# Performance work log

Measured on AMD Instinct MI355X. Metric: run time of the kernel, lower is better.

The kernel has to match this reference:

```python
import jax, jax.numpy as jnp
import numpy as np
from jax.ops import segment_sum, segment_max

DIM = 32   # hidden dim (hardcoded in Net)
N = 10000  # nodes
E = 160000 # edges
B = 64     # graphs in batch


def setup_inputs():
    key = jax.random.key(0)
    ks = jax.random.split(key, 16)
    r = lambda k, s: jax.random.normal(k, s, dtype=jnp.float32) * 0.1
    z = lambda s: jnp.zeros(s, jnp.float32)
    return {
        "x": jax.random.normal(ks[0], (N, 1), jnp.float32),
        "edge_attr": jax.random.normal(ks[1], (E, 2), jnp.float32),
        "lin0_w": r(ks[2], (1, DIM)), "lin0_b": z((DIM,)),
        "nn_w1": r(ks[3], (2, 128)), "nn_b1": z((128,)),
        "nn_w2": r(ks[4], (128, DIM * DIM)), "nn_b2": z((DIM * DIM,)),
        "conv_root": r(ks[5], (DIM, DIM)), "conv_bias": z((DIM,)),
        "gru_w_ih": r(ks[6], (DIM, 3 * DIM)), "gru_w_hh": r(ks[7], (DIM, 3 * DIM)),
        "gru_b_ih": z((3 * DIM,)), "gru_b_hh": z((3 * DIM,)),
        "lstm_w_ih": r(ks[8], (2 * DIM, 4 * DIM)), "lstm_w_hh": r(ks[9], (DIM, 4 * DIM)),
        "lstm_b_ih": z((4 * DIM,)), "lstm_b_hh": z((4 * DIM,)),
        "lin1_w": r(ks[10], (2 * DIM, DIM)), "lin1_b": z((DIM,)),
        "lin2_w": r(ks[11], (DIM, 1)), "lin2_b": z((1,)),
        "edge_index": jax.random.randint(ks[12], (2, E), 0, N),
        "batch": jnp.sort(jax.random.randint(ks[13], (N,), 0, B)),
    }


def _forward(x, edge_attr, params, edge_index, batch):
    (lin0_w, lin0_b, nn_w1, nn_b1, nn_w2, nn_b2, conv_root, conv_bias,
     gru_w_ih, gru_w_hh, gru_b_ih, gru_b_hh,
     lstm_w_ih, lstm_w_hh, lstm_b_ih, lstm_b_hh,
     lin1_w, lin1_b, lin2_w, lin2_b) = params
    src, dst = edge_index[0], edge_index[1]
    deg = jnp.maximum(segment_sum(jnp.ones((E,), x.dtype), dst, num_segments=N), 1.0)[:, None]
    # edge-conditioned weight matrices (depend only on edge_attr -> compute once)
    ew = (jax.nn.relu(edge_attr @ nn_w1 + nn_b1) @ nn_w2 + nn_b2).reshape(E, DIM, DIM)

    out = jax.nn.relu(x @ lin0_w + lin0_b)  # (N, DIM)
    h = out                                  # GRU hidden state
    for _ in range(3):
        # NNConv: gather -> per-edge matmul -> scatter-mean, plus root weight + bias
        msg = jnp.einsum('ei,eio->eo', out[src], ew)          # (E, DIM)
        agg = segment_sum(msg, dst, num_segments=N) / deg      # (N, DIM)
        m = jax.nn.relu(agg + out @ conv_root + conv_bias)
        # single GRU step (seq_len = 1)
        gi = m @ gru_w_ih + gru_b_ih
        gh = h @ gru_w_hh + gru_b_hh
        i_r, i_z, i_n = jnp.split(gi, 3, axis=-1)
        h_r, h_z, h_n = jnp.split(gh, 3, axis=-1)
        rg = jax.nn.sigmoid(i_r + h_r)
        zg = jax.nn.sigmoid(i_z + h_z)
        ng = jnp.tanh(i_n + rg * h_n)
        h = (1.0 - zg) * ng + zg * h
        out = h

    # Set2Set pooling, 3 processing steps
    q_star = jnp.zeros((B, 2 * DIM), x.dtype)
    hh = jnp.zeros((B, DIM), x.dtype)
    cc = jnp.zeros((B, DIM), x.dtype)
    for _ in range(3):
        gates = q_star @ lstm_w_ih + lstm_b_ih + hh @ lstm_w_hh + lstm_b_hh
        ig, fg, gg, og = jnp.split(gates, 4, axis=-1)  # torch gate order i,f,g,o
        cc = jax.nn.sigmoid(fg) * cc + jax.nn.sigmoid(ig) * jnp.tanh(gg)
        hh = jax.nn.sigmoid(og) * jnp.tanh(cc)
        q = hh                                          # (B, DIM)
        e = jnp.sum(out * q[batch], axis=-1)            # (N,)
        a = jnp.exp(e - segment_max(e, batch, num_segments=B)[batch])
        a = a / segment_sum(a, batch, num_segments=B)[batch]
        rvec = segment_sum(a[:, None] * out, batch, num_segments=B)  # (B, DIM)
        q_star = jnp.concatenate([q, rvec], axis=-1)

    y = jax.nn.relu(q_star @ lin1_w + lin1_b)
    return (y @ lin2_w + lin2_b).reshape(-1)  # (B,)


def reference(x, edge_attr, lin0_w, lin0_b, nn_w1, nn_b1, nn_w2, nn_b2, conv_root, conv_bias, gru_w_ih, gru_w_hh, gru_b_ih, gru_b_hh, lstm_w_ih, lstm_w_hh, lstm_b_ih, lstm_b_hh, lin1_w, lin1_b, lin2_w, lin2_b, edge_index, batch):
    params = (lin0_w, lin0_b, nn_w1, nn_b1, nn_w2, nn_b2, conv_root, conv_bias,
              gru_w_ih, gru_w_hh, gru_b_ih, gru_b_hh,
              lstm_w_ih, lstm_w_hh, lstm_b_ih, lstm_b_hh,
              lin1_w, lin1_b, lin2_w, lin2_b)
    return _forward(x, edge_attr, params, edge_index, batch)
```

## Files before the change

kernel.cpp:

```cpp
#include <hip/hip_runtime.h>
#include <math.h>

#define NN 10000
#define NE 160000
#define NG 64
#define DIM 32
#define CAP 96
#define NBIN (CAP + 1)

typedef __attribute__((ext_vector_type(8))) short bf16x8;
typedef __attribute__((ext_vector_type(4))) float f32x4;

__device__ __forceinline__ float sigmoidf_(float x) { return 1.f / (1.f + expf(-x)); }

__device__ __forceinline__ unsigned short f2bf(float x) {
    unsigned u = __float_as_uint(x);
    u += 0x7FFF + ((u >> 16) & 1);
    return (unsigned short)(u >> 16);
}
__device__ __forceinline__ float bf2f(unsigned short b) {
    return __uint_as_float(((unsigned)b) << 16);
}
__device__ __forceinline__ float rlanef(float v, int i) {
    return __uint_as_float((unsigned)__builtin_amdgcn_readlane((int)__float_as_uint(v), i));
}

__global__ void k_setup(const float* __restrict__ w2, unsigned short* __restrict__ w2f,
                        const float* __restrict__ x, const float* __restrict__ lw,
                        const float* __restrict__ lb, float* __restrict__ out,
                        const int* __restrict__ batch, int* __restrict__ gstart,
                        const int* __restrict__ ei, const float* __restrict__ ea,
                        int* __restrict__ cursor,
                        int* __restrict__ srt_src, float* __restrict__ srt_ea) {
    int b = blockIdx.x, t = threadIdx.x;
    if (b < 512) {
        int tid = b * 256 + t;
        int h = tid >> 10, rem = tid & 1023, i = rem >> 5, n = rem & 31;
        float v = w2[tid];
        unsigned short hi = f2bf(v);
        unsigned short lo = f2bf(v - bf2f(hi));
        int s = h >> 5, hm = h & 31, q = hm >> 3, j = hm & 7;
        int tile = n >> 4, nn = n & 15, lane = q * 16 + nn;
        int c = (i * 4 + s) * 2 + tile;
        w2f[(c * 2 + 0) * 512 + lane * 8 + j] = hi;
        w2f[(c * 2 + 1) * 512 + lane * 8 + j] = lo;
    } else if (b < 1762) {
        int idx = (b - 512) * 256 + t;
        int n = idx >> 5, d = idx & 31;
        out[idx] = fmaxf(x[n] * lw[d] + lb[d], 0.f);
    } else if (b == 1762) {
        if (t <= NG) {
            int g = t, lo = 0, hi = NN;
            while (lo < hi) { int mid = (lo + hi) >> 1; if (batch[mid] < g) lo = mid + 1; else hi = mid; }
            gstart[g] = lo;
        }
    } else {
        int e = (b - 1763) * 256 + t;
        if (e < NE) {
            int d = ei[NE + e];
            int p = atomicAdd(&cursor[d], 1);
            int pos = d * CAP + p;
            srt_src[pos] = ei[e];
            srt_ea[2 * pos]     = ea[2 * e];
            srt_ea[2 * pos + 1] = ea[2 * e + 1];
        }
    }
}

__global__ __launch_bounds__(1024) void k_perm(const int* __restrict__ cursor,
                                               int* __restrict__ perm) {
    __shared__ int hist[NBIN * 16];
    __shared__ int binsum[NBIN];
    __shared__ int base[NBIN];
    int t = threadIdx.x;
    for (int i = t; i < NBIN * 16; i += 1024) hist[i] = 0;
    __syncthreads();
    int sub = t & 15;
    for (int n = t; n < NN; n += 1024) {
        int d = cursor[n]; d = d > CAP ? CAP : d;
        atomicAdd(&hist[d * 16 + sub], 1);
    }
    __syncthreads();
    if (t < NBIN) {
        int s = 0;
        #pragma unroll
        for (int k = 0; k < 16; ++k) s += hist[t * 16 + k];
        binsum[t] = s;
    }
    __syncthreads();
    if (t == 0) {
        int acc = 0;
        for (int d = CAP; d >= 0; --d) { base[d] = acc; acc += binsum[d]; }
    }
    __syncthreads();
    if (t < NBIN) {
        int acc = base[t];
        #pragma unroll
        for (int k = 0; k < 16; ++k) {
            int c = hist[t * 16 + k];
            hist[t * 16 + k] = acc;
            acc += c;
        }
    }
    __syncthreads();
    for (int n = t; n < NN; n += 1024) {
        int d = cursor[n]; d = d > CAP ? CAP : d;
        int pos = atomicAdd(&hist[d * 16 + sub], 1);
        perm[pos] = n;
    }
}

#define NS 1040
#define PS 8320
__global__ __launch_bounds__(1024, 8) void k_conv_gru(
    const int* __restrict__ perm,
    const int* __restrict__ cursor, const int* __restrict__ srt_src,
    const float* __restrict__ srt_ea,
    const float* __restrict__ w1, const float* __restrict__ b1,
    const unsigned short* __restrict__ w2f, const float* __restrict__ b2,
    const float* __restrict__ out_old,
    const float* __restrict__ root, const float* __restrict__ cbias,
    const float* __restrict__ wih, const float* __restrict__ whh,
    const float* __restrict__ bih, const float* __restrict__ bhh,
    float* __restrict__ out_new)
{
    __shared__ __align__(16) unsigned short RB[2 * PS];
    __shared__ float sSg[8][DIM];
    __shared__ int sNode[8];
    int t = threadIdx.x;
    int w = t >> 6, lane = t & 63;
    int nslot = w & 7, hhalf = w >> 3;
    int n = perm[blockIdx.x * 8 + nslot];
    if (hhalf == 0 && lane == 0) sNode[nslot] = n;
    int hb = hhalf * 64;

    float acc[32];
    #pragma unroll
    for (int q = 0; q < 32; ++q) acc[q] = 0.f;
    float sacc = 0.f;

    float w1a = w1[hb + lane], w1c = w1[128 + hb + lane], bb = b1[hb + lane];

    int deg = cursor[n];
    int rs = n * CAP;
    const float2* eap = (const float2*)srt_ea;

    int msrc = 0; float mex = 0.f, mey = 0.f;
    if (lane < deg) {
        msrc = srt_src[rs + lane];
        float2 a = eap[rs + lane];
        mex = a.x; mey = a.y;
    }

    int dmain = deg < 64 ? deg : 64;
    int i = 0;
    for (; i + 1 < dmain; i += 2) {
        int s0 = __builtin_amdgcn_readlane(msrc, i);
        int s1 = __builtin_amdgcn_readlane(msrc, i + 1);
        float a0x = rlanef(mex, i),     a0y = rlanef(mey, i);
        float a1x = rlanef(mex, i + 1), a1y = rlanef(mey, i + 1);
        const float* o0 = out_old + s0 * DIM;
        const float* o1 = out_old + s1 * DIM;
        float r0 = fmaxf(a0x * w1a + a0y * w1c + bb, 0.f);
        float r1 = fmaxf(a1x * w1a + a1y * w1c + bb, 0.f);
        #pragma unroll
        for (int q = 0; q < 32; ++q) acc[q] += r0 * o0[q];
        #pragma unroll
        for (int q = 0; q < 32; ++q) acc[q] += r1 * o1[q];
        if (hhalf == 0) {
            const float* oc = (lane < 32) ? (o0 + lane) : (o1 + lane - 32);
            sacc += *oc;
        }
    }
    if (i < dmain) {
        int s0 = __builtin_amdgcn_readlane(msrc, i);
        float a0x = rlanef(mex, i), a0y = rlanef(mey, i);
        const float* o0 = out_old + s0 * DIM;
        float r0 = fmaxf(a0x * w1a + a0y * w1c + bb, 0.f);
        #pragma unroll
        for (int q = 0; q < 32; ++q) acc[q] += r0 * o0[q];
        if (hhalf == 0 && lane < 32) sacc += o0[lane];
    }
    for (int p = rs + 64; p < rs + deg; ++p) {
        int s0 = __builtin_amdgcn_readfirstlane(srt_src[p]);
        float2 a0 = eap[p];
        const float* o0 = out_old + s0 * DIM;
        float r0 = fmaxf(a0.x * w1a + a0.y * w1c + bb, 0.f);
        #pragma unroll
        for (int q = 0; q < 32; ++q) acc[q] += r0 * o0[q];
        if (hhalf == 0 && lane < 32) sacc += o0[lane];
    }
    if (hhalf == 0) {
        sacc += __shfl_xor(sacc, 32);
        if (lane < DIM) sSg[nslot][lane] = sacc;
    }

    int quad = lane >> 4;
    unsigned aoff = (unsigned)((lane & 7) * NS + nslot * 128 + quad * 8);
    f32x4 acc0 = {0.f, 0.f, 0.f, 0.f};
    f32x4 acc1 = {0.f, 0.f, 0.f, 0.f};

    unsigned short* Hw = RB + nslot * NS + hb;
    unsigned short* Lw = RB + PS + nslot * NS + hb;

    #pragma unroll
    for (int pass = 0; pass < 4; ++pass) {
        if (pass) __syncthreads();
        #pragma unroll
        for (int li = 0; li < 8; ++li) {
            float v = acc[pass * 8 + li];
            unsigned short h0 = f2bf(v);
            unsigned short l0 = f2bf(v - bf2f(h0));
            Hw[li * 128 + lane] = h0;
            Lw[li * 128 + lane] = l0;
        }
        __syncthreads();
        int ig = pass * 8 + nslot;
        #pragma unroll
        for (int si = 0; si < 2; ++si) {
            int s = hhalf * 2 + si;
            bf16x8 ah = *(const bf16x8*)(RB + aoff + s * 32);
            bf16x8 al = *(const bf16x8*)(RB + PS + aoff + s * 32);
            const unsigned short* bp = w2f + (unsigned)((ig * 4 + s) * 2048 + lane * 8);
            bf16x8 bh0 = *(const bf16x8*)(bp);
            bf16x8 bl0 = *(const bf16x8*)(bp + 512);
            bf16x8 bh1 = *(const bf16x8*)(bp + 1024);
            bf16x8 bl1 = *(const bf16x8*)(bp + 1536);
            acc0 = __builtin_amdgcn_mfma_f32_16x16x32_bf16(ah, bh0, acc0, 0, 0, 0);
            acc0 = __builtin_amdgcn_mfma_f32_16x16x32_bf16(ah, bl0, acc0, 0, 0, 0);
            acc0 = __builtin_amdgcn_mfma_f32_16x16x32_bf16(al, bh0, acc0, 0, 0, 0);
            acc1 = __builtin_amdgcn_mfma_f32_16x16x32_bf16(ah, bh1, acc1, 0, 0, 0);
            acc1 = __builtin_amdgcn_mfma_f32_16x16x32_bf16(ah, bl1, acc1, 0, 0, 0);
            acc1 = __builtin_amdgcn_mfma_f32_16x16x32_bf16(al, bh1, acc1, 0, 0, 0);
        }
    }
    __syncthreads();

    float* part = (float*)RB;
    #pragma unroll
    for (int r = 0; r < 4; ++r) {
        part[((w * 2 + 0) * 64 + lane) * 4 + r] = acc0[r];
        part[((w * 2 + 1) * 64 + lane) * 4 + r] = acc1[r];
    }
    __syncthreads();

    if (t < 256) {
        int nb = t >> 5, d = t & 31;
        int nn_ = sNode[nb];
        int base = t & 32;
        int tile = d >> 4, col = d & 15;
        int lidx = (nb >> 2) * 16 + col, reg = nb & 3;
        float aggv = 0.f;
        #pragma unroll
        for (int wv = 0; wv < 16; ++wv)
            aggv += part[((wv * 2 + tile) * 64 + lidx) * 4 + reg];

        float bt = 0.f;
        #pragma unroll 8
        for (int i2 = 0; i2 < DIM; ++i2) bt += sSg[nb][i2] * b2[i2 * DIM + d];
        int cdeg = cursor[nn_];
        float degf = (float)(cdeg > 0 ? cdeg : 1);
        aggv = (aggv + bt) / degf;

        float x = out_old[nn_ * DIM + d];
        float rootsum = 0.f;
        #pragma unroll 8
        for (int k = 0; k < DIM; ++k)
            rootsum += __shfl(x, base + k) * root[k * DIM + d];
        float m = fmaxf(aggv + rootsum + cbias[d], 0.f);

        float gir = bih[d], giz = bih[DIM + d], gin = bih[2 * DIM + d];
        float ghr = bhh[d], ghz = bhh[DIM + d], ghn = bhh[2 * DIM + d];
        #pragma unroll 4
        for (int k = 0; k < DIM; ++k) {
            float mk = __shfl(m, base + k);
            float hk = __shfl(x, base + k);
            gir += mk * wih[k * 96 + d];
            giz += mk * wih[k * 96 + DIM + d];
            gin += mk * wih[k * 96 + 2 * DIM + d];
            ghr += hk * whh[k * 96 + d];
            ghz += hk * whh[k * 96 + DIM + d];
            ghn += hk * whh[k * 96 + 2 * DIM + d];
        }
        float rg = sigmoidf_(gir + ghr);
        float zg = sigmoidf_(giz + ghz);
        float ng = tanhf(gin + rg * ghn);
        out_new[nn_ * DIM + d] = (1.f - zg) * ng + zg * x;
    }
}

__global__ __launch_bounds__(256) void k_set2set(
    const float* __restrict__ out, const int* __restrict__ gstart,
    const float* __restrict__ wih, const float* __restrict__ whh,
    const float* __restrict__ bih, const float* __restrict__ bhh,
    const float* __restrict__ l1w, const float* __restrict__ l1b,
    const float* __restrict__ l2w, const float* __restrict__ l2b,
    float* __restrict__ ebuf, float* __restrict__ y)
{
    __shared__ float swih[64 * 128];
    __shared__ float swhh[32 * 128];
    __shared__ float sq[2 * DIM];
    __shared__ float shh[DIM], scc[DIM];
    __shared__ float sgates[4 * DIM];
    __shared__ float sacc[8][DIM];
    __shared__ float sredA[4], sredB[4];

    int g = blockIdx.x, t = threadIdx.x;
    {
        const float4* wv = (const float4*)wih;   float4* sv = (float4*)swih;
        for (int i = t; i < 2048; i += 256) sv[i] = wv[i];
        const float4* wv2 = (const float4*)whh;  float4* sv2 = (float4*)swhh;
        for (int i = t; i < 1024; i += 256) sv2[i] = wv2[i];
    }
    if (t < 2 * DIM) sq[t] = 0.f;
    if (t < DIM) { shh[t] = 0.f; scc[t] = 0.f; }
    int ns = gstart[g], ne = gstart[g + 1];
    __syncthreads();

    for (int step = 0; step < 3; ++step) {
        if (t < 128) {
            float acc = bih[t] + bhh[t];
            #pragma unroll 8
            for (int k = 0; k < 2 * DIM; ++k) acc += sq[k] * swih[k * 128 + t];
            #pragma unroll 8
            for (int k = 0; k < DIM; ++k)     acc += shh[k] * swhh[k * 128 + t];
            sgates[t] = acc;
        }
        __syncthreads();
        if (t < DIM) {
            float ig = sigmoidf_(sgates[t]);
            float fg = sigmoidf_(sgates[DIM + t]);
            float gg = tanhf(sgates[2 * DIM + t]);
            float og = sigmoidf_(sgates[3 * DIM + t]);
            float c_new = fg * scc[t] + ig * gg;
            float h_new = og * tanhf(c_new);
            scc[t] = c_new;
            shh[t] = h_new;
            sq[t] = h_new;
        }
        __syncthreads();

        float lmax = -3.0e38f;
        for (int n = ns + t; n < ne; n += 256) {
            const float4* orow = (const float4*)(out + n * DIM);
            float e = 0.f;
            #pragma unroll
            for (int q = 0; q < 8; ++q) {
                float4 o4 = orow[q];
                e += o4.x * shh[4 * q] + o4.y * shh[4 * q + 1]
                   + o4.z * shh[4 * q + 2] + o4.w * shh[4 * q + 3];
            }
            ebuf[n] = e;
            lmax = fmaxf(lmax, e);
        }
        #pragma unroll
        for (int s = 1; s < 64; s <<= 1) lmax = fmaxf(lmax, __shfl_xor(lmax, s));
        if ((t & 63) == 0) sredA[t >> 6] = lmax;
        __syncthreads();
        float M = fmaxf(fmaxf(sredA[0], sredA[1]), fmaxf(sredA[2], sredA[3]));

        float lsum = 0.f;
        for (int n = ns + t; n < ne; n += 256) {
            float v = expf(ebuf[n] - M);
            ebuf[n] = v;
            lsum += v;
        }
        #pragma unroll
        for (int s = 1; s < 64; s <<= 1) lsum += __shfl_xor(lsum, s);
        if ((t & 63) == 0) sredB[t >> 6] = lsum;
        __syncthreads();
        float S = sredB[0] + sredB[1] + sredB[2] + sredB[3];
        float inv = (S > 0.f) ? 1.f / S : 0.f;

        int stp = t >> 5, d = t & 31;
        float racc = 0.f;
        for (int n = ns + stp; n < ne; n += 8)
            racc += ebuf[n] * out[n * DIM + d];
        sacc[stp][d] = racc;
        __syncthreads();
        if (t < DIM) {
            float r = 0.f;
            #pragma unroll
            for (int s = 0; s < 8; ++s) r += sacc[s][t];
            sq[DIM + t] = r * inv;
        }
        __syncthreads();
    }

    if (t < DIM) {
        float h = l1b[t];
        #pragma unroll 8
        for (int k = 0; k < 2 * DIM; ++k) h += sq[k] * l1w[k * DIM + t];
        float v = fmaxf(h, 0.f) * l2w[t];
        #pragma unroll
        for (int s = 1; s < 32; s <<= 1) v += __shfl_xor(v, s);
        if (t == 0) y[g] = v + l2b[0];
    }
}

extern "C" void kernel_launch(void* const* d_in, const int* in_sizes, int n_in,
                              void* d_out, int out_size, void* d_ws, size_t ws_size,
                              hipStream_t stream) {
    const float* x         = (const float*)d_in[0];
    const float* edge_attr = (const float*)d_in[1];
    const float* lin0_w    = (const float*)d_in[2];
    const float* lin0_b    = (const float*)d_in[3];
    const float* nn_w1     = (const float*)d_in[4];
    const float* nn_b1     = (const float*)d_in[5];
    const float* nn_w2     = (const float*)d_in[6];
    const float* nn_b2     = (const float*)d_in[7];
    const float* conv_root = (const float*)d_in[8];
    const float* conv_bias = (const float*)d_in[9];
    const float* gru_w_ih  = (const float*)d_in[10];
    const float* gru_w_hh  = (const float*)d_in[11];
    const float* gru_b_ih  = (const float*)d_in[12];
    const float* gru_b_hh  = (const float*)d_in[13];
    const float* lstm_w_ih = (const float*)d_in[14];
    const float* lstm_w_hh = (const float*)d_in[15];
    const float* lstm_b_ih = (const float*)d_in[16];
    const float* lstm_b_hh = (const float*)d_in[17];
    const float* lin1_w    = (const float*)d_in[18];
    const float* lin1_b    = (const float*)d_in[19];
    const float* lin2_w    = (const float*)d_in[20];
    const float* lin2_b    = (const float*)d_in[21];
    const int*   edge_index= (const int*)d_in[22];
    const int*   batch     = (const int*)d_in[23];
    float* yout = (float*)d_out;

    char* p = (char*)d_ws;
    auto alloc = [&](size_t bytes) { char* r = p; p += (bytes + 255) & ~(size_t)255; return r; };

    int*   cursor = (int*)  alloc(NN * sizeof(int));
    size_t zero_bytes = (size_t)(p - (char*)d_ws);
    int*   gstart    = (int*)  alloc((NG + 1) * sizeof(int));
    int*   srt_src   = (int*)  alloc((size_t)NN * CAP * sizeof(int));
    float* srt_ea    = (float*)alloc((size_t)NN * CAP * 2 * sizeof(float));
    float* outA      = (float*)alloc(NN * DIM * sizeof(float));
    float* outB      = (float*)alloc(NN * DIM * sizeof(float));
    int*   perm      = (int*)  alloc(NN * sizeof(int));
    unsigned short* w2f = (unsigned short*)alloc(262144 * sizeof(unsigned short));
    float* ebuf      = (float*)alloc(NN * sizeof(float));
    (void)ws_size; (void)n_in; (void)in_sizes; (void)out_size;

    hipMemsetAsync(d_ws, 0, zero_bytes, stream);

    k_setup<<<2388, 256, 0, stream>>>(nn_w2, w2f, x, lin0_w, lin0_b, outA, batch, gstart,
                                      edge_index, edge_attr, cursor, srt_src, srt_ea);
    k_perm<<<1, 1024, 0, stream>>>(cursor, perm);

    const float* cur = outA;
    float* nxt = outB;
    for (int it = 0; it < 3; ++it) {
        k_conv_gru<<<1250, 1024, 0, stream>>>(perm, cursor, srt_src, srt_ea,
                                              nn_w1, nn_b1, w2f, nn_b2,
                                              cur,
                                              conv_root, conv_bias,
                                              gru_w_ih, gru_w_hh, gru_b_ih, gru_b_hh,
                                              nxt);
        const float* tmp = nxt; nxt = (float*)cur; cur = tmp;
    }
    const float* outF = cur;

    k_set2set<<<NG, 256, 0, stream>>>(outF, gstart,
                                      lstm_w_ih, lstm_w_hh, lstm_b_ih, lstm_b_hh,
                                      lin1_w, lin1_b, lin2_w, lin2_b, ebuf, yout);
}
```

Baseline: 330.0 us.

## Compute per-node edge-hidden by input aggregation with split-bf16 MFMA

Replaces the scalar per-edge FMA loop, which accumulated relu(edge MLP hidden) times the gathered source features into 32 registers per lane, with MFMA tiles. Edges are processed in chunks of 32: source indices and edge attributes are spread with ds_bpermute, features and hidden activations are split into hi/lo bf16 pairs, and four MFMAs per tile keep near-fp32 accuracy. The LDS staging layout is changed to match the new accumulator ownership, with a larger padded stride, and the launch-bounds occupancy hint drops from 8 to 4. This trades scalar VALU work for extra conversion and bpermute overhead. The lower occupancy hint may reduce latency hiding, and the fallback path for degree above 64 still runs scalar code.

New measurement: 396.9 us. +20.3%, slower.

```diff
diff --git a/kernel.cpp b/kernel.cpp
--- a/kernel.cpp
+++ b/kernel.cpp
@@ -21,8 +21,13 @@
 __device__ __forceinline__ float bf2f(unsigned short b) {
     return __uint_as_float(((unsigned)b) << 16);
 }
-__device__ __forceinline__ float rlanef(float v, int i) {
-    return __uint_as_float((unsigned)__builtin_amdgcn_readlane((int)__float_as_uint(v), i));
+__device__ __forceinline__ float bpermf(int addr, float v) {
+    return __uint_as_float((unsigned)__builtin_amdgcn_ds_bpermute(addr, (int)__float_as_uint(v)));
+}
+__device__ __forceinline__ bf16x8 mk8(unsigned a, unsigned b, unsigned c, unsigned d) {
+    union { unsigned u[4]; bf16x8 v; } x;
+    x.u[0] = a; x.u[1] = b; x.u[2] = c; x.u[3] = d;
+    return x.v;
 }
 
 __global__ void k_setup(const float* __restrict__ w2, unsigned short* __restrict__ w2f,
@@ -110,9 +115,9 @@
     }
 }
 
-#define NS 1040
-#define PS 8320
-__global__ __launch_bounds__(1024, 8) void k_conv_gru(
+#define NS 1104
+#define PS (8 * NS)
+__global__ __launch_bounds__(1024, 4) void k_conv_gru(
     const int* __restrict__ perm,
     const int* __restrict__ cursor, const int* __restrict__ srt_src,
     const float* __restrict__ srt_ea,
@@ -129,17 +134,11 @@
     __shared__ int sNode[8];
     int t = threadIdx.x;
     int w = t >> 6, lane = t & 63;
-    int nslot = w & 7, hhalf = w >> 3;
+    int nslot = w & 7, hh = w >> 3;
     int n = perm[blockIdx.x * 8 + nslot];
-    if (hhalf == 0 && lane == 0) sNode[nslot] = n;
-    int hb = hhalf * 64;
-
-    float acc[32];
-    #pragma unroll
-    for (int q = 0; q < 32; ++q) acc[q] = 0.f;
-    float sacc = 0.f;
-
-    float w1a = w1[hb + lane], w1c = w1[128 + hb + lane], bb = b1[hb + lane];
+    if (hh == 0 && lane == 0) sNode[nslot] = n;
+    int hb = hh * 64;
+    int grp = lane >> 4, glan = lane & 15;
 
     int deg = cursor[n];
     int rs = n * CAP;
@@ -152,73 +151,149 @@
         mex = a.x; mey = a.y;
     }
 
+    float w1a_[4], w1c_[4], b1_[4];
+    #pragma unroll
+    for (int ht = 0; ht < 4; ++ht) {
+        int hx = hb + ht * 16 + glan;
+        w1a_[ht] = w1[hx]; w1c_[ht] = w1[128 + hx]; b1_[ht] = b1[hx];
+    }
+
+    f32x4 racc[4][2];
+    #pragma unroll
+    for (int ht = 0; ht < 4; ++ht) {
+        #pragma unroll
+        for (int it = 0; it < 2; ++it) racc[ht][it] = (f32x4){0.f, 0.f, 0.f, 0.f};
+    }
+    float sg0 = 0.f, sg1 = 0.f;
+
     int dmain = deg < 64 ? deg : 64;
-    int i = 0;
-    for (; i + 1 < dmain; i += 2) {
-        int s0 = __builtin_amdgcn_readlane(msrc, i);
-        int s1 = __builtin_amdgcn_readlane(msrc, i + 1);
-        float a0x = rlanef(mex, i),     a0y = rlanef(mey, i);
-        float a1x = rlanef(mex, i + 1), a1y = rlanef(mey, i + 1);
-        const float* o0 = out_old + s0 * DIM;
-        const float* o1 = out_old + s1 * DIM;
-        float r0 = fmaxf(a0x * w1a + a0y * w1c + bb, 0.f);
-        float r1 = fmaxf(a1x * w1a + a1y * w1c + bb, 0.f);
-        #pragma unroll
-        for (int q = 0; q < 32; ++q) acc[q] += r0 * o0[q];
-        #pragma unroll
-        for (int q = 0; q < 32; ++q) acc[q] += r1 * o1[q];
-        if (hhalf == 0) {
-            const float* oc = (lane < 32) ? (o0 + lane) : (o1 + lane - 32);
-            sacc += *oc;
-        }
-    }
-    if (i < dmain) {
-        int s0 = __builtin_amdgcn_readlane(msrc, i);
-        float a0x = rlanef(mex, i), a0y = rlanef(mey, i);
-        const float* o0 = out_old + s0 * DIM;
-        float r0 = fmaxf(a0x * w1a + a0y * w1c + bb, 0.f);
-        #pragma unroll
-        for (int q = 0; q < 32; ++q) acc[q] += r0 * o0[q];
-        if (hhalf == 0 && lane < 32) sacc += o0[lane];
-    }
-    for (int p = rs + 64; p < rs + deg; ++p) {
-        int s0 = __builtin_amdgcn_readfirstlane(srt_src[p]);
-        float2 a0 = eap[p];
-        const float* o0 = out_old + s0 * DIM;
-        float r0 = fmaxf(a0.x * w1a + a0.y * w1c + bb, 0.f);
-        #pragma unroll
-        for (int q = 0; q < 32; ++q) acc[q] += r0 * o0[q];
-        if (hhalf == 0 && lane < 32) sacc += o0[lane];
-    }
-    if (hhalf == 0) {
-        sacc += __shfl_xor(sacc, 32);
-        if (lane < DIM) sSg[nslot][lane] = sacc;
-    }
-
-    int quad = lane >> 4;
-    unsigned aoff = (unsigned)((lane & 7) * NS + nslot * 128 + quad * 8);
+    int nks = (dmain + 31) >> 5;
+    for (int ks = 0; ks < nks; ++ks) {
+        int sj[8]; float ex[8], ey[8];
+        #pragma unroll
+        for (int j = 0; j < 8; ++j) {
+            int e = ks * 32 + grp * 8 + j;
+            int ba = e << 2;
+            sj[j] = __builtin_amdgcn_ds_bpermute(ba, msrc);
+            ex[j] = bpermf(ba, mex);
+            ey[j] = bpermf(ba, mey);
+        }
+        float xv0[8], xv1[8];
+        #pragma unroll
+        for (int j = 0; j < 8; ++j) {
+            const float* rp = out_old + sj[j] * DIM;
+            xv0[j] = rp[glan];
+            xv1[j] = rp[16 + glan];
+        }
+        #pragma unroll
+        for (int j = 0; j < 8; ++j) {
+            int e = ks * 32 + grp * 8 + j;
+            if (e >= deg) { xv0[j] = 0.f; xv1[j] = 0.f; }
+        }
+        if (hh == 0) {
+            float s0_ = ((xv0[0]+xv0[1])+(xv0[2]+xv0[3]))+((xv0[4]+xv0[5])+(xv0[6]+xv0[7]));
+            float s1_ = ((xv1[0]+xv1[1])+(xv1[2]+xv1[3]))+((xv1[4]+xv1[5])+(xv1[6]+xv1[7]));
+            s0_ += __shfl_xor(s0_, 16); s0_ += __shfl_xor(s0_, 32);
+            s1_ += __shfl_xor(s1_, 16); s1_ += __shfl_xor(s1_, 32);
+            sg0 += s0_; sg1 += s1_;
+        }
+        unsigned ph0[4], pl0[4], ph1[4], pl1[4];
+        #pragma unroll
+        for (int j2 = 0; j2 < 4; ++j2) {
+            unsigned short hA = f2bf(xv0[2*j2]),  hB = f2bf(xv0[2*j2+1]);
+            unsigned short lA = f2bf(xv0[2*j2] - bf2f(hA)), lB = f2bf(xv0[2*j2+1] - bf2f(hB));
+            ph0[j2] = (unsigned)hA | ((unsigned)hB << 16);
+            pl0[j2] = (unsigned)lA | ((unsigned)lB << 16);
+            unsigned short hC = f2bf(xv1[2*j2]),  hD = f2bf(xv1[2*j2+1]);
+            unsigned short lC = f2bf(xv1[2*j2] - bf2f(hC)), lD = f2bf(xv1[2*j2+1] - bf2f(hD));
+            ph1[j2] = (unsigned)hC | ((unsigned)hD << 16);
+            pl1[j2] = (unsigned)lC | ((unsigned)lD << 16);
+        }
+        bf16x8 xbh0 = mk8(ph0[0], ph0[1], ph0[2], ph0[3]);
+        bf16x8 xbl0 = mk8(pl0[0], pl0[1], pl0[2], pl0[3]);
+        bf16x8 xbh1 = mk8(ph1[0], ph1[1], ph1[2], ph1[3]);
+        bf16x8 xbl1 = mk8(pl1[0], pl1[1], pl1[2], pl1[3]);
+
+        #pragma unroll
+        for (int ht = 0; ht < 4; ++ht) {
+            float rv[8];
+            #pragma unroll
+            for (int j = 0; j < 8; ++j)
+                rv[j] = fmaxf(ex[j] * w1a_[ht] + ey[j] * w1c_[ht] + b1_[ht], 0.f);
+            unsigned ah_[4], al_[4];
+            #pragma unroll
+            for (int j2 = 0; j2 < 4; ++j2) {
+                unsigned short hA = f2bf(rv[2*j2]),  hB = f2bf(rv[2*j2+1]);
+                unsigned short lA = f2bf(rv[2*j2] - bf2f(hA)), lB = f2bf(rv[2*j2+1] - bf2f(hB));
+                ah_[j2] = (unsigned)hA | ((unsigned)hB << 16);
+                al_[j2] = (unsigned)lA | ((unsigned)lB << 16);
+            }
+            bf16x8 rah = mk8(ah_[0], ah_[1], ah_[2], ah_[3]);
+            bf16x8 ral = mk8(al_[0], al_[1], al_[2], al_[3]);
+            racc[ht][0] = __builtin_amdgcn_mfma_f32_16x16x32_bf16(rah, xbh0, racc[ht][0], 0, 0, 0);
+            racc[ht][0] = __builtin_amdgcn_mfma_f32_16x16x32_bf16(rah, xbl0, racc[ht][0], 0, 0, 0);
+            racc[ht][0] = __builtin_amdgcn_mfma_f32_16x16x32_bf16(ral, xbh0, racc[ht][0], 0, 0, 0);
+            racc[ht][0] = __builtin_amdgcn_mfma_f32_16x16x32_bf16(ral, xbl0, racc[ht][0], 0, 0, 0);
+            racc[ht][1] = __builtin_amdgcn_mfma_f32_16x16x32_bf16(rah, xbh1, racc[ht][1], 0, 0, 0);
+            racc[ht][1] = __builtin_amdgcn_mfma_f32_16x16x32_bf16(rah, xbl1, racc[ht][1], 0, 0, 0);
+            racc[ht][1] = __builtin_amdgcn_mfma_f32_16x16x32_bf16(ral, xbh1, racc[ht][1], 0, 0, 0);
+            racc[ht][1] = __builtin_amdgcn_mfma_f32_16x16x32_bf16(ral, xbl1, racc[ht][1], 0, 0, 0);
+        }
+    }
+    if (deg > 64) {
+        for (int p2 = rs + 64; p2 < rs + deg; ++p2) {
+            int s0 = __builtin_amdgcn_readfirstlane(srt_src[p2]);
+            float2 a0 = eap[p2];
+            float xi0 = out_old[s0 * DIM + glan];
+            float xi1 = out_old[s0 * DIM + 16 + glan];
+            #pragma unroll
+            for (int ht = 0; ht < 4; ++ht) {
+                #pragma unroll
+                for (int rr = 0; rr < 4; ++rr) {
+                    int hx = hb + ht * 16 + grp * 4 + rr;
+                    float rh_ = fmaxf(a0.x * w1[hx] + a0.y * w1[128 + hx] + b1[hx], 0.f);
+                    racc[ht][0][rr] += rh_ * xi0;
+                    racc[ht][1][rr] += rh_ * xi1;
+                }
+            }
+            if (hh == 0) { sg0 += xi0; sg1 += xi1; }
+        }
+    }
+    if (hh == 0 && grp == 0) {
+        sSg[nslot][glan] = sg0;
+        sSg[nslot][16 + glan] = sg1;
+    }
+
     f32x4 acc0 = {0.f, 0.f, 0.f, 0.f};
     f32x4 acc1 = {0.f, 0.f, 0.f, 0.f};
-
-    unsigned short* Hw = RB + nslot * NS + hb;
-    unsigned short* Lw = RB + PS + nslot * NS + hb;
+    unsigned aoff = (unsigned)((lane & 7) * NS + nslot * 136 + grp * 8);
+    int myhalf = (lane >> 3) & 1;
 
     #pragma unroll
     for (int pass = 0; pass < 4; ++pass) {
         if (pass) __syncthreads();
-        #pragma unroll
-        for (int li = 0; li < 8; ++li) {
-            float v = acc[pass * 8 + li];
-            unsigned short h0 = f2bf(v);
-            unsigned short l0 = f2bf(v - bf2f(h0));
-            Hw[li * 128 + lane] = h0;
-            Lw[li * 128 + lane] = l0;
+        if (myhalf == (pass & 1)) {
+            int li = lane & 7;
+            unsigned short* Hp = RB + (unsigned)(nslot * NS + li * 136);
+            unsigned short* Lp = Hp + PS;
+            #pragma unroll
+            for (int ht = 0; ht < 4; ++ht) {
+                #pragma unroll
+                for (int rr = 0; rr < 4; ++rr) {
+                    float v = racc[ht][pass >> 1][rr];
+                    int hx = hb + ht * 16 + grp * 4 + rr;
+                    unsigned short h0 = f2bf(v);
+                    unsigned short l0 = f2bf(v - bf2f(h0));
+                    Hp[hx] = h0;
+                    Lp[hx] = l0;
+                }
+            }
         }
         __syncthreads();
         int ig = pass * 8 + nslot;
         #pragma unroll
         for (int si = 0; si < 2; ++si) {
-            int s = hhalf * 2 + si;
+            int s = hh * 2 + si;
             bf16x8 ah = *(const bf16x8*)(RB + aoff + s * 32);
             bf16x8 al = *(const bf16x8*)(RB + PS + aoff + s * 32);
             const unsigned short* bp = w2f + (unsigned)((ig * 4 + s) * 2048 + lane * 8);
```
